# Optimization experiments

Hardware: AMD Instinct MI355X
Metric: run time of the kernel (lower is better)

## Reference

```python
import jax, jax.numpy as jnp
import numpy as np

# ---- module hyperparams (match init_kwargs) ----
IN_CH, OUT_CH = 32, 64
KERNEL = 9
STRIDE, PADDING = 1, 4
GRID_SIZE, SPLINE_ORDER = 5, 3
GRID_LO, GRID_HI = -1.0, 1.0
NUM_COEF = GRID_SIZE + SPLINE_ORDER  # 8 spline basis functions


def make_grid():
    h = (GRID_HI - GRID_LO) / GRID_SIZE
    # extended knot vector, same for every input feature (efficient-KAN)
    return (jnp.arange(-SPLINE_ORDER, GRID_SIZE + SPLINE_ORDER + 1, dtype=jnp.float32) * h + GRID_LO)


def b_splines(x, grid, order):
    """Cox-de Boor B-spline bases. x: (...,) -> (..., NUM_COEF)."""
    x = x[..., None]
    bases = ((x >= grid[:-1]) & (x < grid[1:])).astype(x.dtype)
    for k in range(1, order + 1):
        left = (x - grid[: -(k + 1)]) / (grid[k:-1] - grid[: -(k + 1)])
        right = (grid[k + 1:] - x) / (grid[k + 1:] - grid[1:-k])
        bases = left * bases[..., :-1] + right * bases[..., 1:]
    return bases


def setup_inputs() -> dict:
    key = jax.random.key(0)
    k1, k2, k3, k4 = jax.random.split(key, 4)
    x = jax.random.normal(k1, (16, IN_CH, 2048), dtype=jnp.float32)
    # all O*I KANLinear(kernel->1) modules batched into single tensors
    base_w = jax.random.normal(k2, (OUT_CH, IN_CH, KERNEL), dtype=jnp.float32) * (1.0 / np.sqrt(KERNEL))
    spline_w = jax.random.normal(k3, (OUT_CH, IN_CH, KERNEL, NUM_COEF), dtype=jnp.float32) * 0.1
    spline_scaler = jax.random.normal(k4, (OUT_CH, IN_CH, KERNEL), dtype=jnp.float32) * (1.0 / np.sqrt(KERNEL))
    return {"x": x, "base_w": base_w, "spline_w": spline_w, "spline_scaler": spline_scaler}


def reference(x, base_w, spline_w, spline_scaler):
    grid = make_grid()
    B, I, L = x.shape
    L_out = (L + 2 * PADDING - (KERNEL - 1) - 1) // STRIDE + 1  # dilation=1
    xp = jnp.pad(x, ((0, 0), (0, 0), (PADDING, PADDING)))
    # sliding windows: (B, I, L_out, K)
    idx = jnp.arange(L_out)[:, None] * STRIDE + jnp.arange(KERNEL)[None, :]
    win = xp[:, :, idx]
    # base branch: silu(window) . base_weight, summed over in_channels
    out = jnp.einsum('bilk,oik->bol', jax.nn.silu(win), base_w)
    # spline branch
    bs = b_splines(win, grid, SPLINE_ORDER)          # (B, I, L_out, K, C)
    sw = spline_w * spline_scaler[..., None]         # scaled spline weight
    out = out + jnp.einsum('bilkc,oikc->bol', bs, sw)
    return out
```

## Files before the change

kernel.cpp:

```cpp
#include <hip/hip_runtime.h>
#include <hip/hip_bf16.h>

namespace {

constexpr int KIN  = 32;
constexpr int KOUT = 64;
constexpr int KW   = 9;
constexpr int KPAD = 4;
constexpr int LIN  = 2048;
constexpr int KTOT = 2592;
constexpr int NCH  = 81;

typedef __bf16 bf16x8 __attribute__((ext_vector_type(8)));
typedef float  f32x4  __attribute__((ext_vector_type(4)));

__device__ __forceinline__ unsigned short f2bf(float x) {
    unsigned int u = __float_as_uint(x);
    u += 0x7FFFu + ((u >> 16) & 1u);
    return (unsigned short)(u >> 16);
}

__global__ __launch_bounds__(256) void kan_wprep(const float* __restrict__ base_w,
                                                 const float* __restrict__ spline_w,
                                                 const float* __restrict__ spline_scaler,
                                                 unsigned short* __restrict__ Wf) {
    int t = blockIdx.x * 256 + threadIdx.x;
    if (t >= KOUT * KIN * KW) return;
    int k = t % KW;
    int i = (t / KW) % KIN;
    int o = t / (KW * KIN);
    float sc = spline_scaler[t];
    int m  = o >> 4;
    int lo = o & 15;
#pragma unroll
    for (int c = 0; c < 9; ++c) {
        float val = (c == 0) ? base_w[t] : spline_w[(size_t)t * 8 + (c - 1)] * sc;
        int kappa = k * 288 + i * 9 + c;
        int ch = kappa >> 5;
        int hi = (kappa & 31) >> 3;
        int e  = kappa & 7;
        Wf[((size_t)(ch * 4 + m) * 64 + hi * 16 + lo) * 8 + e] = f2bf(val);
    }
}

constexpr int BN     = 64;
constexpr int TROW   = 72;
constexpr int F2COLS = 296;

__global__ __launch_bounds__(256, 2) void kan_fused(const float* __restrict__ x,
                                                    const unsigned short* __restrict__ Wf,
                                                    float* __restrict__ out) {
    __shared__ char smem[65536];
    unsigned short* f2t = (unsigned short*)smem;
    float*          red = (float*)smem;

    int tid  = threadIdx.x;
    int lane = tid & 63;
    int wv   = tid >> 6;
    int lo = lane & 15, hi = lane >> 4;

    int blk = blockIdx.x;
    int b   = blk >> 5;
    int l0  = (blk & 31) * BN;

    {
        f32x4 z = (f32x4){0.f, 0.f, 0.f, 0.f};
        for (int c = tid; c < TROW * F2COLS / 8; c += 256)
            *(f32x4*)(f2t + (size_t)c * 8) = z;
    }
    __syncthreads();

#pragma unroll
    for (int pass = 0; pass < 9; ++pass) {
        int unit = pass * 256 + tid;
        int i = unit / TROW;
        int r = unit - i * TROW;
        int gx = l0 + r - KPAD;
        float v = 0.f;
        if (gx >= 0 && gx < LIN) v = x[((size_t)b * KIN + i) * LIN + gx];
        unsigned short* row = f2t + (size_t)r * F2COLS + i * 9;
        row[0] = f2bf(v / (1.f + __expf(-v)));
        float t5 = (v + 2.2f) * 2.5f;
        float mf = floorf(t5);
        int   m  = (int)mf;
        float u  = t5 - mf;
        float u2 = u * u, u3 = u2 * u;
        float w  = 1.f - u;
        float P0 = u3 * (1.f / 6.f);
        float P3 = w * w * w * (1.f / 6.f);
        float P1 = (1.f / 6.f) + 0.5f * u + 0.5f * u2 - 0.5f * u3;
        float P2 = (4.f / 6.f) - u2 + 0.5f * u3;
        int c0 = m - 3;
        if ((unsigned)(c0 + 0) <= 7u) row[1 + c0 + 0] = f2bf(P3);
        if ((unsigned)(c0 + 1) <= 7u) row[1 + c0 + 1] = f2bf(P2);
        if ((unsigned)(c0 + 2) <= 7u) row[1 + c0 + 2] = f2bf(P1);
        if ((unsigned)(c0 + 3) <= 7u) row[1 + c0 + 3] = f2bf(P0);
    }
    __syncthreads();

    int nch = (wv == 0) ? 21 : 20;
    int ch0 = (wv == 0) ? 0 : wv * 20 + 1;

    f32x4 acc[4][4];
#pragma unroll
    for (int m = 0; m < 4; ++m)
#pragma unroll
        for (int n = 0; n < 4; ++n) acc[m][n] = (f32x4){0.f, 0.f, 0.f, 0.f};

    const unsigned short* wbase = Wf + (size_t)lane * 8;
    const unsigned short* fbase = f2t + (size_t)lo * F2COLS + hi * 8;

    int ch = ch0;
    int kk = ch / 9, jb = ch - kk * 9;
    bf16x8 av[4], bv[4];
#pragma unroll
    for (int m = 0; m < 4; ++m)
        av[m] = *(const bf16x8*)(wbase + (size_t)(ch * 4 + m) * 512);
#pragma unroll
    for (int n = 0; n < 4; ++n)
        bv[n] = *(const bf16x8*)(fbase + (size_t)(n * 16 + kk) * F2COLS + jb * 32);

    for (int t = 0; t < nch; ++t) {
        int chn = (t + 1 < nch) ? ch + 1 : ch;
        int kn = chn / 9, jbn = chn - kn * 9;
        bf16x8 an[4], bn[4];
#pragma unroll
        for (int m = 0; m < 4; ++m)
            an[m] = *(const bf16x8*)(wbase + (size_t)(chn * 4 + m) * 512);
#pragma unroll
        for (int n = 0; n < 4; ++n)
            bn[n] = *(const bf16x8*)(fbase + (size_t)(n * 16 + kn) * F2COLS + jbn * 32);
#pragma unroll
        for (int m = 0; m < 4; ++m)
#pragma unroll
            for (int n = 0; n < 4; ++n)
                acc[m][n] = __builtin_amdgcn_mfma_f32_16x16x32_bf16(av[m], bv[n], acc[m][n], 0, 0, 0);
#pragma unroll
        for (int m = 0; m < 4; ++m) av[m] = an[m];
#pragma unroll
        for (int n = 0; n < 4; ++n) bv[n] = bn[n];
        ch = chn;
    }

    __syncthreads();
    {
        float* myp = red + (size_t)wv * 4096;
#pragma unroll
        for (int m = 0; m < 4; ++m)
#pragma unroll
            for (int n = 0; n < 4; ++n)
                *(f32x4*)(myp + ((size_t)(m * 4 + n) * 64 + lane) * 4) = acc[m][n];
    }
    __syncthreads();

#pragma unroll
    for (int n = 0; n < 4; ++n) {
        int p = wv * 4 + n;
        f32x4 s = (f32x4){0.f, 0.f, 0.f, 0.f};
#pragma unroll
        for (int w = 0; w < 4; ++w)
            s += *(const f32x4*)(red + (size_t)w * 4096 + ((size_t)p * 64 + lane) * 4);
        float* op = out + ((size_t)b * KOUT + wv * 16 + hi * 4) * LIN + l0 + n * 16 + lo;
#pragma unroll
        for (int r = 0; r < 4; ++r) op[(size_t)r * LIN] = s[r];
    }
}

}

extern "C" void kernel_launch(void* const* d_in, const int* in_sizes, int n_in,
                              void* d_out, int out_size, void* d_ws, size_t ws_size,
                              hipStream_t stream) {
    const float* x             = (const float*)d_in[0];
    const float* base_w        = (const float*)d_in[1];
    const float* spline_w      = (const float*)d_in[2];
    const float* spline_scaler = (const float*)d_in[3];
    float* out = (float*)d_out;

    unsigned short* Wf = (unsigned short*)d_ws;

    kan_wprep<<<(KOUT * KIN * KW + 255) / 256, 256, 0, stream>>>(base_w, spline_w, spline_scaler, Wf);
    kan_fused<<<512, 256, 0, stream>>>(x, Wf, out);
}
```

Measured before the change: 25.79 us.

## Use 512-thread blocks with 8-wave K split and two-phase reduction

Doubles the block to 8 waves, so each wave covers about 10 K-chunks of the MFMA loop instead of 20, and the feature-tile build loop drops from 9 passes to 5. The explicit register double-buffering is replaced with direct loads, pointer increments and s_setprio around the MFMA group. The cross-wave reduction runs in two phases through the 64KB LDS buffer to fit 8 waves' partial sums. The aim is more latency hiding per block, paid for with a larger reduction, an extra barrier, and less explicit prefetch.

```diff
diff --git a/kernel.cpp b/kernel.cpp
--- a/kernel.cpp
+++ b/kernel.cpp
@@ -9,7 +9,6 @@
 constexpr int KPAD = 4;
 constexpr int LIN  = 2048;
 constexpr int KTOT = 2592;
-constexpr int NCH  = 81;
 
 typedef __bf16 bf16x8 __attribute__((ext_vector_type(8)));
 typedef float  f32x4  __attribute__((ext_vector_type(4)));
@@ -47,7 +46,7 @@
 constexpr int TROW   = 72;
 constexpr int F2COLS = 296;
 
-__global__ __launch_bounds__(256, 2) void kan_fused(const float* __restrict__ x,
+__global__ __launch_bounds__(512, 4) void kan_fused(const float* __restrict__ x,
                                                     const unsigned short* __restrict__ Wf,
                                                     float* __restrict__ out) {
     __shared__ char smem[65536];
@@ -65,41 +64,44 @@
 
     {
         f32x4 z = (f32x4){0.f, 0.f, 0.f, 0.f};
-        for (int c = tid; c < TROW * F2COLS / 8; c += 256)
+        for (int c = tid; c < TROW * F2COLS / 8; c += 512)
             *(f32x4*)(f2t + (size_t)c * 8) = z;
     }
     __syncthreads();
 
 #pragma unroll
-    for (int pass = 0; pass < 9; ++pass) {
-        int unit = pass * 256 + tid;
+    for (int pass = 0; pass < 5; ++pass) {
+        int unit = pass * 512 + tid;
+        bool ok = unit < TROW * KIN;
         int i = unit / TROW;
         int r = unit - i * TROW;
         int gx = l0 + r - KPAD;
         float v = 0.f;
-        if (gx >= 0 && gx < LIN) v = x[((size_t)b * KIN + i) * LIN + gx];
-        unsigned short* row = f2t + (size_t)r * F2COLS + i * 9;
-        row[0] = f2bf(v / (1.f + __expf(-v)));
-        float t5 = (v + 2.2f) * 2.5f;
-        float mf = floorf(t5);
-        int   m  = (int)mf;
-        float u  = t5 - mf;
-        float u2 = u * u, u3 = u2 * u;
-        float w  = 1.f - u;
-        float P0 = u3 * (1.f / 6.f);
-        float P3 = w * w * w * (1.f / 6.f);
-        float P1 = (1.f / 6.f) + 0.5f * u + 0.5f * u2 - 0.5f * u3;
-        float P2 = (4.f / 6.f) - u2 + 0.5f * u3;
-        int c0 = m - 3;
-        if ((unsigned)(c0 + 0) <= 7u) row[1 + c0 + 0] = f2bf(P3);
-        if ((unsigned)(c0 + 1) <= 7u) row[1 + c0 + 1] = f2bf(P2);
-        if ((unsigned)(c0 + 2) <= 7u) row[1 + c0 + 2] = f2bf(P1);
-        if ((unsigned)(c0 + 3) <= 7u) row[1 + c0 + 3] = f2bf(P0);
+        if (ok && gx >= 0 && gx < LIN) v = x[((size_t)b * KIN + i) * LIN + gx];
+        if (ok) {
+            unsigned short* row = f2t + (size_t)r * F2COLS + i * 9;
+            row[0] = f2bf(v / (1.f + __expf(-v)));
+            float t5 = (v + 2.2f) * 2.5f;
+            float mf = floorf(t5);
+            int   m  = (int)mf;
+            float u  = t5 - mf;
+            float u2 = u * u, u3 = u2 * u;
+            float w  = 1.f - u;
+            float P0 = u3 * (1.f / 6.f);
+            float P3 = w * w * w * (1.f / 6.f);
+            float P1 = (1.f / 6.f) + 0.5f * u + 0.5f * u2 - 0.5f * u3;
+            float P2 = (4.f / 6.f) - u2 + 0.5f * u3;
+            int c0 = m - 3;
+            if ((unsigned)(c0 + 0) <= 7u) row[1 + c0 + 0] = f2bf(P3);
+            if ((unsigned)(c0 + 1) <= 7u) row[1 + c0 + 1] = f2bf(P2);
+            if ((unsigned)(c0 + 2) <= 7u) row[1 + c0 + 2] = f2bf(P1);
+            if ((unsigned)(c0 + 3) <= 7u) row[1 + c0 + 3] = f2bf(P0);
+        }
     }
     __syncthreads();
 
-    int nch = (wv == 0) ? 21 : 20;
-    int ch0 = (wv == 0) ? 0 : wv * 20 + 1;
+    int nch = (wv == 0) ? 11 : 10;
+    int ch0 = (wv == 0) ? 0 : 10 * wv + 1;
 
     f32x4 acc[4][4];
 #pragma unroll
@@ -107,62 +109,67 @@
 #pragma unroll
         for (int n = 0; n < 4; ++n) acc[m][n] = (f32x4){0.f, 0.f, 0.f, 0.f};
 
-    const unsigned short* wbase = Wf + (size_t)lane * 8;
-    const unsigned short* fbase = f2t + (size_t)lo * F2COLS + hi * 8;
-
-    int ch = ch0;
-    int kk = ch / 9, jb = ch - kk * 9;
-    bf16x8 av[4], bv[4];
-#pragma unroll
-    for (int m = 0; m < 4; ++m)
-        av[m] = *(const bf16x8*)(wbase + (size_t)(ch * 4 + m) * 512);
-#pragma unroll
-    for (int n = 0; n < 4; ++n)
-        bv[n] = *(const bf16x8*)(fbase + (size_t)(n * 16 + kk) * F2COLS + jb * 32);
+    int kk = ch0 / 9;
+    int jb = ch0 - kk * 9;
+    const unsigned short* wptr = Wf + (size_t)ch0 * 2048 + (size_t)lane * 8;
+    const unsigned short* fptr = f2t + (size_t)(lo + kk) * F2COLS + jb * 32 + hi * 8;
 
     for (int t = 0; t < nch; ++t) {
-        int chn = (t + 1 < nch) ? ch + 1 : ch;
-        int kn = chn / 9, jbn = chn - kn * 9;
-        bf16x8 an[4], bn[4];
-#pragma unroll
-        for (int m = 0; m < 4; ++m)
-            an[m] = *(const bf16x8*)(wbase + (size_t)(chn * 4 + m) * 512);
-#pragma unroll
-        for (int n = 0; n < 4; ++n)
-            bn[n] = *(const bf16x8*)(fbase + (size_t)(n * 16 + kn) * F2COLS + jbn * 32);
-#pragma unroll
-        for (int m = 0; m < 4; ++m)
-#pragma unroll
-            for (int n = 0; n < 4; ++n)
-                acc[m][n] = __builtin_amdgcn_mfma_f32_16x16x32_bf16(av[m], bv[n], acc[m][n], 0, 0, 0);
-#pragma unroll
-        for (int m = 0; m < 4; ++m) av[m] = an[m];
-#pragma unroll
-        for (int n = 0; n < 4; ++n) bv[n] = bn[n];
-        ch = chn;
+        bf16x8 a0 = *(const bf16x8*)(wptr);
+        bf16x8 a1 = *(const bf16x8*)(wptr + 512);
+        bf16x8 a2 = *(const bf16x8*)(wptr + 1024);
+        bf16x8 a3 = *(const bf16x8*)(wptr + 1536);
+        bf16x8 b0 = *(const bf16x8*)(fptr);
+        bf16x8 b1 = *(const bf16x8*)(fptr + 16 * F2COLS);
+        bf16x8 b2 = *(const bf16x8*)(fptr + 32 * F2COLS);
+        bf16x8 b3 = *(const bf16x8*)(fptr + 48 * F2COLS);
+        __builtin_amdgcn_s_setprio(1);
+        acc[0][0] = __builtin_amdgcn_mfma_f32_16x16x32_bf16(a0, b0, acc[0][0], 0, 0, 0);
+        acc[0][1] = __builtin_amdgcn_mfma_f32_16x16x32_bf16(a0, b1, acc[0][1], 0, 0, 0);
+        acc[0][2] = __builtin_amdgcn_mfma_f32_16x16x32_bf16(a0, b2, acc[0][2], 0, 0, 0);
+        acc[0][3] = __builtin_amdgcn_mfma_f32_16x16x32_bf16(a0, b3, acc[0][3], 0, 0, 0);
+        acc[1][0] = __builtin_amdgcn_mfma_f32_16x16x32_bf16(a1, b0, acc[1][0], 0, 0, 0);
+        acc[1][1] = __builtin_amdgcn_mfma_f32_16x16x32_bf16(a1, b1, acc[1][1], 0, 0, 0);
+        acc[1][2] = __builtin_amdgcn_mfma_f32_16x16x32_bf16(a1, b2, acc[1][2], 0, 0, 0);
+        acc[1][3] = __builtin_amdgcn_mfma_f32_16x16x32_bf16(a1, b3, acc[1][3], 0, 0, 0);
+        acc[2][0] = __builtin_amdgcn_mfma_f32_16x16x32_bf16(a2, b0, acc[2][0], 0, 0, 0);
+        acc[2][1] = __builtin_amdgcn_mfma_f32_16x16x32_bf16(a2, b1, acc[2][1], 0, 0, 0);
+        acc[2][2] = __builtin_amdgcn_mfma_f32_16x16x32_bf16(a2, b2, acc[2][2], 0, 0, 0);
+        acc[2][3] = __builtin_amdgcn_mfma_f32_16x16x32_bf16(a2, b3, acc[2][3], 0, 0, 0);
+        acc[3][0] = __builtin_amdgcn_mfma_f32_16x16x32_bf16(a3, b0, acc[3][0], 0, 0, 0);
+        acc[3][1] = __builtin_amdgcn_mfma_f32_16x16x32_bf16(a3, b1, acc[3][1], 0, 0, 0);
+        acc[3][2] = __builtin_amdgcn_mfma_f32_16x16x32_bf16(a3, b2, acc[3][2], 0, 0, 0);
+        acc[3][3] = __builtin_amdgcn_mfma_f32_16x16x32_bf16(a3, b3, acc[3][3], 0, 0, 0);
+        __builtin_amdgcn_s_setprio(0);
+        wptr += 2048;
+        jb += 1;
+        fptr += (jb == 9) ? (F2COLS - 8 * 32) : 32;
+        if (jb == 9) jb = 0;
     }
 
     __syncthreads();
-    {
-        float* myp = red + (size_t)wv * 4096;
 #pragma unroll
-        for (int m = 0; m < 4; ++m)
+    for (int mp = 0; mp < 2; ++mp) {
+#pragma unroll
+        for (int dm = 0; dm < 2; ++dm)
 #pragma unroll
             for (int n = 0; n < 4; ++n)
-                *(f32x4*)(myp + ((size_t)(m * 4 + n) * 64 + lane) * 4) = acc[m][n];
-    }
-    __syncthreads();
-
+                *(f32x4*)(red + (((size_t)wv * 8 + dm * 4 + n) * 64 + lane) * 4) = acc[mp * 2 + dm][n];
+        __syncthreads();
+        {
+            int dm = wv >> 2, n = wv & 3;
+            f32x4 s = (f32x4){0.f, 0.f, 0.f, 0.f};
 #pragma unroll
-    for (int n = 0; n < 4; ++n) {
-        int p = wv * 4 + n;
-        f32x4 s = (f32x4){0.f, 0.f, 0.f, 0.f};
-#pragma unroll
-        for (int w = 0; w < 4; ++w)
-            s += *(const f32x4*)(red + (size_t)w * 4096 + ((size_t)p * 64 + lane) * 4);
-        float* op = out + ((size_t)b * KOUT + wv * 16 + hi * 4) * LIN + l0 + n * 16 + lo;
-#pragma unroll
-        for (int r = 0; r < 4; ++r) op[(size_t)r * LIN] = s[r];
+            for (int w = 0; w < 8; ++w)
+                s += *(const f32x4*)(red + (((size_t)w * 8 + dm * 4 + n) * 64 + lane) * 4);
+            int o = (mp * 2 + dm) * 16 + hi * 4;
+            float* op = out + ((size_t)b * KOUT + o) * LIN + l0 + n * 16 + lo;
+            op[0]          = s[0];
+            op[LIN]        = s[1];
+            op[2 * LIN]    = s[2];
+            op[3 * (size_t)LIN] = s[3];
+        }
+        if (mp == 0) __syncthreads();
     }
 }
 
@@ -180,5 +187,5 @@
     unsigned short* Wf = (unsigned short*)d_ws;
 
     kan_wprep<<<(KOUT * KIN * KW + 255) / 256, 256, 0, stream>>>(base_w, spline_w, spline_scaler, Wf);
-    kan_fused<<<512, 256, 0, stream>>>(x, Wf, out);
+    kan_fused<<<512, 512, 0, stream>>>(x, Wf, out);
 }
```

Result: faster. 23.12 us (-10.3%).
